# Kernel tuning notes

Measured on AMD Instinct MI355X. Metric: run time of the kernel, lower is better.

The kernel has to match this reference:

```python
import jax, jax.numpy as jnp
import numpy as np

NUM_LAYERS, B, S, H = 2, 32, 4096, 1024
NEG_INF = -1.0e9


def setup_inputs() -> dict:
    key = jax.random.key(0)
    k1, k2, k3 = jax.random.split(key, 3)
    hidden = jax.random.normal(k1, (NUM_LAYERS, B, H), dtype=jnp.float32)
    encoder_outputs = jax.random.normal(k2, (B, S, H), dtype=jnp.float32)
    mask = jax.random.randint(k3, (B, S), 0, 2).astype(jnp.bool_)
    return {"hidden": hidden, "encoder_outputs": encoder_outputs, "mask": mask}


def reference(hidden, encoder_outputs, mask):
    # hidden: [L, B, H] -> take last layer [B, H]
    h = hidden[-1]
    # scores: [B, S] = einsum over H
    scores = jnp.einsum("bsh,bh->bs", encoder_outputs, h)
    scores = jnp.where(mask, scores, NEG_INF)
    attn = jax.nn.softmax(scores, axis=1)  # [B, S]
    # context: [B, H]
    context = jnp.einsum("bs,bsh->bh", attn, encoder_outputs)
    return (context, attn)
```

## Files before the change

kernel.cpp:

```cpp
#include <hip/hip_runtime.h>
#include <math.h>

#define B_ 32
#define S_ 4096
#define H_ 1024
#define NBLK 16
#define ROWS_PER_BLOCK (S_ / NBLK)
#define NWAVE 4
#define ROWS_PER_WAVE (ROWS_PER_BLOCK / NWAVE)
#define NEG_INF_ -1.0e9f

__global__ __launch_bounds__(256) void attn_pass1(
    const float* __restrict__ hidden,
    const float* __restrict__ enc,
    const int*   __restrict__ mask,
    float* __restrict__ scores,
    float* __restrict__ part_ctx,
    float* __restrict__ part_ml)
{
    const int blk  = blockIdx.x;
    const int b    = blk / NBLK;
    const int cb   = blk % NBLK;
    const int tid  = threadIdx.x;
    const int wave = tid >> 6;
    const int lane = tid & 63;

    const float4* h4 = (const float4*)(hidden + (size_t)(B_ + b) * H_);
    const float4 hf0 = h4[lane];
    const float4 hf1 = h4[lane + 64];
    const float4 hf2 = h4[lane + 128];
    const float4 hf3 = h4[lane + 192];

    float m = -INFINITY;
    float l = 0.0f;
    float4 c0 = {0.f, 0.f, 0.f, 0.f};
    float4 c1 = c0, c2 = c0, c3 = c0;
    float myscore = 0.0f;

    const int    row0  = cb * ROWS_PER_BLOCK + wave * ROWS_PER_WAVE;
    const float* encb  = enc  + (size_t)b * S_ * H_;
    const int*   maskb = mask + (size_t)b * S_;

    for (int r = 0; r < ROWS_PER_WAVE; ++r) {
        const int s = row0 + r;
        const float4* row4 = (const float4*)(encb + (size_t)s * H_);
        const float4 r0 = row4[lane];
        const float4 r1 = row4[lane + 64];
        const float4 r2 = row4[lane + 128];
        const float4 r3 = row4[lane + 192];

        float dot = r0.x * hf0.x + r0.y * hf0.y + r0.z * hf0.z + r0.w * hf0.w;
        dot += r1.x * hf1.x + r1.y * hf1.y + r1.z * hf1.z + r1.w * hf1.w;
        dot += r2.x * hf2.x + r2.y * hf2.y + r2.z * hf2.z + r2.w * hf2.w;
        dot += r3.x * hf3.x + r3.y * hf3.y + r3.z * hf3.z + r3.w * hf3.w;

        #pragma unroll
        for (int off = 32; off >= 1; off >>= 1)
            dot += __shfl_xor(dot, off, 64);

        const float score = (maskb[s] != 0) ? dot : NEG_INF_;
        if (r == lane) myscore = score;

        const float newm  = fmaxf(m, score);
        const float scale = __expf(m - newm);
        const float p     = __expf(score - newm);
        l = l * scale + p;
        c0.x = c0.x * scale + p * r0.x;  c0.y = c0.y * scale + p * r0.y;
        c0.z = c0.z * scale + p * r0.z;  c0.w = c0.w * scale + p * r0.w;
        c1.x = c1.x * scale + p * r1.x;  c1.y = c1.y * scale + p * r1.y;
        c1.z = c1.z * scale + p * r1.z;  c1.w = c1.w * scale + p * r1.w;
        c2.x = c2.x * scale + p * r2.x;  c2.y = c2.y * scale + p * r2.y;
        c2.z = c2.z * scale + p * r2.z;  c2.w = c2.w * scale + p * r2.w;
        c3.x = c3.x * scale + p * r3.x;  c3.y = c3.y * scale + p * r3.y;
        c3.z = c3.z * scale + p * r3.z;  c3.w = c3.w * scale + p * r3.w;
        m = newm;
    }

    scores[(size_t)b * S_ + row0 + lane] = myscore;

    __shared__ float lds_ctx[NWAVE][H_];
    __shared__ float lds_m[NWAVE];
    __shared__ float lds_l[NWAVE];
    float4* dst = (float4*)lds_ctx[wave];
    dst[lane]       = c0;
    dst[lane + 64]  = c1;
    dst[lane + 128] = c2;
    dst[lane + 192] = c3;
    if (lane == 0) { lds_m[wave] = m; lds_l[wave] = l; }
    __syncthreads();

    const float M  = fmaxf(fmaxf(lds_m[0], lds_m[1]), fmaxf(lds_m[2], lds_m[3]));
    const float w0 = __expf(lds_m[0] - M);
    const float w1 = __expf(lds_m[1] - M);
    const float w2 = __expf(lds_m[2] - M);
    const float w3 = __expf(lds_m[3] - M);

    const int e = tid * 4;
    const float4 a0 = *(const float4*)&lds_ctx[0][e];
    const float4 a1 = *(const float4*)&lds_ctx[1][e];
    const float4 a2 = *(const float4*)&lds_ctx[2][e];
    const float4 a3 = *(const float4*)&lds_ctx[3][e];
    float4 o;
    o.x = a0.x * w0 + a1.x * w1 + a2.x * w2 + a3.x * w3;
    o.y = a0.y * w0 + a1.y * w1 + a2.y * w2 + a3.y * w3;
    o.z = a0.z * w0 + a1.z * w1 + a2.z * w2 + a3.z * w3;
    o.w = a0.w * w0 + a1.w * w1 + a2.w * w2 + a3.w * w3;
    *(float4*)&part_ctx[(size_t)blk * H_ + e] = o;

    if (tid == 0) {
        const float L = lds_l[0] * w0 + lds_l[1] * w1 + lds_l[2] * w2 + lds_l[3] * w3;
        part_ml[blk * 2]     = M;
        part_ml[blk * 2 + 1] = L;
    }
}

__global__ __launch_bounds__(256) void attn_pass2(
    const float* __restrict__ part_ctx,
    const float* __restrict__ part_ml,
    float* __restrict__ out_ctx,
    float* __restrict__ attn)
{
    const int b    = blockIdx.x;
    const int part = blockIdx.y;
    const int tid  = threadIdx.x;

    float M = -INFINITY;
    #pragma unroll
    for (int p = 0; p < NBLK; ++p)
        M = fmaxf(M, part_ml[(b * NBLK + p) * 2]);

    float w[NBLK];
    float L = 0.0f;
    #pragma unroll
    for (int p = 0; p < NBLK; ++p) {
        w[p] = __expf(part_ml[(b * NBLK + p) * 2] - M);
        L += part_ml[(b * NBLK + p) * 2 + 1] * w[p];
    }
    const float invL = 1.0f / L;

    if (part == 0) {
        const int e = tid * 4;
        float4 acc = {0.f, 0.f, 0.f, 0.f};
        #pragma unroll
        for (int p = 0; p < NBLK; ++p) {
            const float4 v = *(const float4*)&part_ctx[(size_t)(b * NBLK + p) * H_ + e];
            acc.x += v.x * w[p];  acc.y += v.y * w[p];
            acc.z += v.z * w[p];  acc.w += v.w * w[p];
        }
        acc.x *= invL; acc.y *= invL; acc.z *= invL; acc.w *= invL;
        *(float4*)&out_ctx[(size_t)b * H_ + e] = acc;
    } else {
        const size_t s0 = (size_t)b * S_ + (size_t)(part - 1) * 1024 + tid * 4;
        float4 sc = *(const float4*)&attn[s0];
        sc.x = __expf(sc.x - M) * invL;
        sc.y = __expf(sc.y - M) * invL;
        sc.z = __expf(sc.z - M) * invL;
        sc.w = __expf(sc.w - M) * invL;
        *(float4*)&attn[s0] = sc;
    }
}

extern "C" void kernel_launch(void* const* d_in, const int* in_sizes, int n_in,
                              void* d_out, int out_size, void* d_ws, size_t ws_size,
                              hipStream_t stream) {
    (void)in_sizes; (void)n_in; (void)out_size; (void)ws_size;
    const float* hidden = (const float*)d_in[0];
    const float* enc    = (const float*)d_in[1];
    const int*   mask   = (const int*)d_in[2];

    float* out      = (float*)d_out;
    float* out_ctx  = out;
    float* attn     = out + (size_t)B_ * H_;

    float* part_ctx = (float*)d_ws;
    float* part_ml  = part_ctx + (size_t)B_ * NBLK * H_;

    attn_pass1<<<dim3(B_ * NBLK), dim3(256), 0, stream>>>(
        hidden, enc, mask, attn, part_ctx, part_ml);
    attn_pass2<<<dim3(B_, 5), dim3(256), 0, stream>>>(
        part_ctx, part_ml, out_ctx, attn);
}
```

Baseline: 685.6 us.

## Split sequence across more blocks, prefetch next row, and skip unneeded rescales

Raises the sequence split from 16 to 64 blocks per batch so 2048 blocks run instead of 512. Each wave now handles 16 rows instead of 64, and occupancy is hinted with launch_bounds(256,4). Each wave prefetches the next encoder row into registers while it computes the current one, and the online-softmax rescale of the accumulators now runs only when the running max increases. Pass 2 recomputes the merge weights instead of holding them in an array, which adds some work when merging more partials. The score write is guarded so that only the lanes owning a row store.

```diff
diff --git a/kernel.cpp b/kernel.cpp
--- a/kernel.cpp
+++ b/kernel.cpp
@@ -4,13 +4,13 @@
 #define B_ 32
 #define S_ 4096
 #define H_ 1024
-#define NBLK 16
+#define NBLK 64
 #define ROWS_PER_BLOCK (S_ / NBLK)
 #define NWAVE 4
 #define ROWS_PER_WAVE (ROWS_PER_BLOCK / NWAVE)
 #define NEG_INF_ -1.0e9f
 
-__global__ __launch_bounds__(256) void attn_pass1(
+__global__ __launch_bounds__(256, 4) void attn_pass1(
     const float* __restrict__ hidden,
     const float* __restrict__ enc,
     const int*   __restrict__ mask,
@@ -41,13 +41,21 @@
     const float* encb  = enc  + (size_t)b * S_ * H_;
     const int*   maskb = mask + (size_t)b * S_;
 
+    const float4* rp = (const float4*)(encb + (size_t)row0 * H_);
+    float4 n0 = rp[lane];
+    float4 n1 = rp[lane + 64];
+    float4 n2 = rp[lane + 128];
+    float4 n3 = rp[lane + 192];
+
     for (int r = 0; r < ROWS_PER_WAVE; ++r) {
-        const int s = row0 + r;
-        const float4* row4 = (const float4*)(encb + (size_t)s * H_);
-        const float4 r0 = row4[lane];
-        const float4 r1 = row4[lane + 64];
-        const float4 r2 = row4[lane + 128];
-        const float4 r3 = row4[lane + 192];
+        const float4 r0 = n0, r1 = n1, r2 = n2, r3 = n3;
+        if (r + 1 < ROWS_PER_WAVE) {
+            const float4* np = (const float4*)(encb + (size_t)(row0 + r + 1) * H_);
+            n0 = np[lane];
+            n1 = np[lane + 64];
+            n2 = np[lane + 128];
+            n3 = np[lane + 192];
+        }
 
         float dot = r0.x * hf0.x + r0.y * hf0.y + r0.z * hf0.z + r0.w * hf0.w;
         dot += r1.x * hf1.x + r1.y * hf1.y + r1.z * hf1.z + r1.w * hf1.w;
@@ -58,25 +66,29 @@
         for (int off = 32; off >= 1; off >>= 1)
             dot += __shfl_xor(dot, off, 64);
 
+        const int s = row0 + r;
         const float score = (maskb[s] != 0) ? dot : NEG_INF_;
         if (r == lane) myscore = score;
 
-        const float newm  = fmaxf(m, score);
-        const float scale = __expf(m - newm);
-        const float p     = __expf(score - newm);
-        l = l * scale + p;
-        c0.x = c0.x * scale + p * r0.x;  c0.y = c0.y * scale + p * r0.y;
-        c0.z = c0.z * scale + p * r0.z;  c0.w = c0.w * scale + p * r0.w;
-        c1.x = c1.x * scale + p * r1.x;  c1.y = c1.y * scale + p * r1.y;
-        c1.z = c1.z * scale + p * r1.z;  c1.w = c1.w * scale + p * r1.w;
-        c2.x = c2.x * scale + p * r2.x;  c2.y = c2.y * scale + p * r2.y;
-        c2.z = c2.z * scale + p * r2.z;  c2.w = c2.w * scale + p * r2.w;
-        c3.x = c3.x * scale + p * r3.x;  c3.y = c3.y * scale + p * r3.y;
-        c3.z = c3.z * scale + p * r3.z;  c3.w = c3.w * scale + p * r3.w;
-        m = newm;
+        if (score > m) {
+            const float scale = __expf(m - score);
+            l *= scale;
+            c0.x *= scale; c0.y *= scale; c0.z *= scale; c0.w *= scale;
+            c1.x *= scale; c1.y *= scale; c1.z *= scale; c1.w *= scale;
+            c2.x *= scale; c2.y *= scale; c2.z *= scale; c2.w *= scale;
+            c3.x *= scale; c3.y *= scale; c3.z *= scale; c3.w *= scale;
+            m = score;
+        }
+        const float p = __expf(score - m);
+        l += p;
+        c0.x += p * r0.x;  c0.y += p * r0.y;  c0.z += p * r0.z;  c0.w += p * r0.w;
+        c1.x += p * r1.x;  c1.y += p * r1.y;  c1.z += p * r1.z;  c1.w += p * r1.w;
+        c2.x += p * r2.x;  c2.y += p * r2.y;  c2.z += p * r2.z;  c2.w += p * r2.w;
+        c3.x += p * r3.x;  c3.y += p * r3.y;  c3.z += p * r3.z;  c3.w += p * r3.w;
     }
 
-    scores[(size_t)b * S_ + row0 + lane] = myscore;
+    if (lane < ROWS_PER_WAVE)
+        scores[(size_t)b * S_ + row0 + lane] = myscore;
 
     __shared__ float lds_ctx[NWAVE][H_];
     __shared__ float lds_m[NWAVE];
@@ -125,27 +137,26 @@
     const int tid  = threadIdx.x;
 
     float M = -INFINITY;
-    #pragma unroll
+    #pragma unroll 8
     for (int p = 0; p < NBLK; ++p)
         M = fmaxf(M, part_ml[(b * NBLK + p) * 2]);
 
-    float w[NBLK];
     float L = 0.0f;
-    #pragma unroll
-    for (int p = 0; p < NBLK; ++p) {
-        w[p] = __expf(part_ml[(b * NBLK + p) * 2] - M);
-        L += part_ml[(b * NBLK + p) * 2 + 1] * w[p];
-    }
+    #pragma unroll 8
+    for (int p = 0; p < NBLK; ++p)
+        L += part_ml[(b * NBLK + p) * 2 + 1] *
+             __expf(part_ml[(b * NBLK + p) * 2] - M);
     const float invL = 1.0f / L;
 
     if (part == 0) {
         const int e = tid * 4;
         float4 acc = {0.f, 0.f, 0.f, 0.f};
-        #pragma unroll
+        #pragma unroll 4
         for (int p = 0; p < NBLK; ++p) {
+            const float w = __expf(part_ml[(b * NBLK + p) * 2] - M);
             const float4 v = *(const float4*)&part_ctx[(size_t)(b * NBLK + p) * H_ + e];
-            acc.x += v.x * w[p];  acc.y += v.y * w[p];
-            acc.z += v.z * w[p];  acc.w += v.w * w[p];
+            acc.x += v.x * w;  acc.y += v.y * w;
+            acc.z += v.z * w;  acc.w += v.w * w;
         }
         acc.x *= invL; acc.y *= invL; acc.z *= invL; acc.w *= invL;
         *(float4*)&out_ctx[(size_t)b * H_ + e] = acc;
```

New measurement: 698.2 us. No clear change (+1.8%).
